# Optimization experiments

Measured on AMD Instinct MI355X. Metric: run time of the kernel, lower is better.

Reference implementation:

```python
import jax, jax.numpy as jnp
import numpy as np

IN_F, OUT_F = 4096, 11008
IN_G, OUT_G = 8, 1
NUM_CB, CB_SIZE = 2, 256


def setup_inputs() -> dict:
    key = jax.random.key(0)
    k1, k2, k3, k4, k5 = jax.random.split(key, 5)
    no, ni = OUT_F // OUT_G, IN_F // IN_G
    x = jax.random.normal(k1, (4, 2048, IN_F), dtype=jnp.float32)
    codes = jax.random.randint(k2, (no, ni, NUM_CB), 0, CB_SIZE, dtype=jnp.int32)
    codebooks = jax.random.normal(k3, (NUM_CB, CB_SIZE, OUT_G, IN_G), dtype=jnp.float32)
    scales = jax.random.uniform(k4, (no, 1, 1, 1), dtype=jnp.float32) + 0.5
    bias = jax.random.normal(k5, (OUT_F,), dtype=jnp.float32)
    return {"x": x, "codes": codes, "codebooks": codebooks, "scales": scales, "bias": bias}


def _dequantize_weight(codes, codebooks, scales):
    # codes: [no, ni, M] ints; codebooks: [M, C, og, ig]; scales: [no, 1, 1, 1]
    M = codebooks.shape[0]
    og, ig = codebooks.shape[2], codebooks.shape[3]
    no, ni = codes.shape[0], codes.shape[1]
    # gather each codebook's entry and sum over codebooks -> [no, ni, og, ig]
    m_idx = jnp.arange(M)[None, None, :]
    gathered = codebooks[m_idx, codes]            # [no, ni, M, og, ig]
    deq = gathered.sum(axis=2) * scales           # [no, ni, og, ig]
    # reorder groups back to dense weight [out_features, in_features]
    return deq.transpose(0, 2, 1, 3).reshape(no * og, ni * ig)


def reference(x, codes, codebooks, scales, bias):
    w = _dequantize_weight(codes, codebooks, scales)  # [OUT_F, IN_F]
    return jnp.einsum("bsi,oi->bso", x, w) + bias
```

## Files before the change

kernel.cpp:

```cpp
#include <hip/hip_runtime.h>
#include <hip/hip_bf16.h>
#include <stdint.h>

#define IN_F   4096
#define OUT_F  11008
#define M_TOK  8192

typedef __attribute__((ext_vector_type(4))) int   int32x4;

__global__ __launch_bounds__(256) void k_prep(
        const float* __restrict__ x,
        const int* __restrict__ codes,
        const float* __restrict__ codebooks,
        const float* __restrict__ scales,
        signed char* __restrict__ Xq, float* __restrict__ sx,
        signed char* __restrict__ Wq, float* __restrict__ sw) {
    __shared__ float cb[4096];
    __shared__ float red[256];
    int t = threadIdx.x;

    if (blockIdx.x < M_TOK) {
        int r = blockIdx.x;
        const float4* xr = (const float4*)(x + (size_t)r * IN_F) + t * 4;
        float4 v0 = xr[0], v1 = xr[1], v2 = xr[2], v3 = xr[3];
        float m = 0.f;
#define MX4(v) m = fmaxf(m, fmaxf(fmaxf(fabsf(v.x), fabsf(v.y)), fmaxf(fabsf(v.z), fabsf(v.w))))
        MX4(v0); MX4(v1); MX4(v2); MX4(v3);
        red[t] = m; __syncthreads();
        for (int s = 128; s > 0; s >>= 1) {
            if (t < s) red[t] = fmaxf(red[t], red[t + s]);
            __syncthreads();
        }
        float rm = fmaxf(red[0], 1e-8f);
        if (t == 0) sx[r] = rm / 127.f;
        float inv = 127.f / rm;
        union { signed char c[16]; uint4 u; } pk;
#define Q4(v, o) pk.c[o] = (signed char)__float2int_rn(v.x * inv);            \
                 pk.c[o+1] = (signed char)__float2int_rn(v.y * inv);          \
                 pk.c[o+2] = (signed char)__float2int_rn(v.z * inv);          \
                 pk.c[o+3] = (signed char)__float2int_rn(v.w * inv)
        Q4(v0, 0); Q4(v1, 4); Q4(v2, 8); Q4(v3, 12);
        *(uint4*)(Xq + (size_t)r * IN_F + t * 16) = pk.u;
    } else {
        int o = blockIdx.x - M_TOK;
        {
            const float4* cbg = (const float4*)codebooks;
            float4* cbl = (float4*)cb;
#pragma unroll
            for (int i = 0; i < 4; ++i) cbl[t + i * 256] = cbg[t + i * 256];
        }
        __syncthreads();
        const int2* cp = (const int2*)codes + (size_t)o * 512 + t * 2;
        int2 c0 = cp[0], c1 = cp[1];
        float e[16]; float m = 0.f;
#pragma unroll
        for (int j = 0; j < 8; ++j) {
            e[j]     = cb[c0.x * 8 + j] + cb[2048 + c0.y * 8 + j];
            e[8 + j] = cb[c1.x * 8 + j] + cb[2048 + c1.y * 8 + j];
        }
#pragma unroll
        for (int j = 0; j < 16; ++j) m = fmaxf(m, fabsf(e[j]));
        red[t] = m; __syncthreads();
        for (int s = 128; s > 0; s >>= 1) {
            if (t < s) red[t] = fmaxf(red[t], red[t + s]);
            __syncthreads();
        }
        float rm = fmaxf(red[0], 1e-8f);
        if (t == 0) sw[o] = scales[o] * rm / 127.f;
        float inv = 127.f / rm;
        union { signed char c[16]; uint4 u; } pk;
#pragma unroll
        for (int j = 0; j < 16; ++j) pk.c[j] = (signed char)__float2int_rn(e[j] * inv);
        *(uint4*)(Wq + (size_t)o * IN_F + t * 16) = pk.u;
    }
}


#define BARRIER() __builtin_amdgcn_s_barrier()
#define VMW(n)    asm volatile("s_waitcnt vmcnt(" #n ")")

#define GL16(gp, lp) __builtin_amdgcn_global_load_lds(                        \
    (const __attribute__((address_space(1))) void*)(gp),                      \
    (__attribute__((address_space(3))) void*)(lp), 16, 0, 0)

__global__ __launch_bounds__(512, 2) void k_gemm(
        const signed char* __restrict__ A,
        const signed char* __restrict__ B,
        const float* __restrict__ sx,
        const float* __restrict__ sw,
        const float* __restrict__ bias,
        float* __restrict__ out) {
    __shared__ signed char lA0[256 * 128];
    __shared__ signed char lA1[256 * 128];
    __shared__ signed char lB0[256 * 128];
    __shared__ signed char lB1[256 * 128];

    const int tid = threadIdx.x;
    const int l = tid & 63;
    const int w = tid >> 6;
    const int wm = w >> 2, wn = w & 3;

    int lid = blockIdx.x;
    int xcd = lid & 7, j = lid >> 3;
    int bx = j >> 2;
    int by = (xcd << 2) + (j & 3);
    const int rowBase = by * 256;
    const int colBase = bx * 256;

    const int srow = w * 8 + (l >> 3);
    const int scol = ((l & 7) ^ ((l >> 3) & 7)) << 4;
    const signed char* gA = A + (size_t)(rowBase + srow) * IN_F + scol;
    const signed char* gB = B + (size_t)(colBase + srow) * IN_F + scol;
    signed char* lA0w = &lA0[w * 8 * 128];
    signed char* lA1w = &lA1[w * 8 * 128];
    signed char* lB0w = &lB0[w * 8 * 128];
    signed char* lB1w = &lB1[w * 8 * 128];

#define STAGEQ_(P, t, q) do {                                                 \
    const signed char* _g = (((q) < 2) ? gA : gB) + (size_t)(t) * 128;        \
    signed char* _l = (((q) < 2) ? lA##P##w : lB##P##w);                      \
    const int _r = ((q) & 1) * 128;                                           \
    GL16(_g + (size_t)_r * IN_F,        _l + _r * 128);                       \
    GL16(_g + (size_t)(_r + 64) * IN_F, _l + (_r + 64) * 128);                \
} while (0)

    const int frow = l & 15, g = l >> 4;
    const int cho0 = ((g ^ (frow & 7)) << 4);
    const int cho1 = (((4 + g) ^ (frow & 7)) << 4);
    const char* rowA0 = (const char*)&lA0[(wm * 128 + frow) * 128];
    const char* rowA1 = (const char*)&lA1[(wm * 128 + frow) * 128];
    const char* rowB0 = (const char*)&lB0[(wn * 64 + frow) * 128];
    const char* rowB1 = (const char*)&lB1[(wn * 64 + frow) * 128];
#define LDA_(P, m, kk) (*(const int32x4*)(rowA##P + (m) * 2048 + ((kk) ? cho1 : cho0)))
#define LDB_(P, n, kk) (*(const int32x4*)(rowB##P + (n) * 2048 + ((kk) ? cho1 : cho0)))

    int32x4 acc[8][4] = {};
    int32x4 ar[4][2], br[4][2];

#define QUAD(M0, N0) do {                                                     \
    _Pragma("unroll") for (int mm = 0; mm < 4; ++mm)                          \
    _Pragma("unroll") for (int nn = 0; nn < 2; ++nn)                          \
    _Pragma("unroll") for (int kk = 0; kk < 2; ++kk)                          \
        acc[(M0) + mm][(N0) + nn] = __builtin_amdgcn_mfma_i32_16x16x64_i8(    \
            ar[mm][kk], br[(N0) + nn][kk], acc[(M0) + mm][(N0) + nn], 0, 0, 0);\
} while (0)

#define RD_A03_B01(P) do {                                                    \
    _Pragma("unroll") for (int mm = 0; mm < 4; ++mm) {                        \
        ar[mm][0] = LDA_(P, mm, 0); ar[mm][1] = LDA_(P, mm, 1); }             \
    br[0][0] = LDB_(P, 0, 0); br[0][1] = LDB_(P, 0, 1);                       \
    br[1][0] = LDB_(P, 1, 0); br[1][1] = LDB_(P, 1, 1);                       \
} while (0)
#define RD_B23(P) do {                                                        \
    br[2][0] = LDB_(P, 2, 0); br[2][1] = LDB_(P, 2, 1);                       \
    br[3][0] = LDB_(P, 3, 0); br[3][1] = LDB_(P, 3, 1);                       \
} while (0)
#define RD_A47(P) do {                                                        \
    _Pragma("unroll") for (int mm = 0; mm < 4; ++mm) {                        \
        ar[mm][0] = LDA_(P, 4 + mm, 0); ar[mm][1] = LDA_(P, 4 + mm, 1); }     \
} while (0)

    STAGEQ_(0, 0, 0); STAGEQ_(0, 0, 1); STAGEQ_(0, 0, 2); STAGEQ_(0, 0, 3);
    STAGEQ_(1, 1, 2); STAGEQ_(1, 1, 3); STAGEQ_(1, 1, 0); STAGEQ_(1, 1, 1);
    VMW(8); BARRIER();

    for (int i = 0; i < 15; ++i) {
        int t = 2 * i;
        RD_A03_B01(0);
        QUAD(0, 0); BARRIER();
        RD_B23(0);
        QUAD(0, 2); BARRIER();
        RD_A47(0); STAGEQ_(0, t + 2, 2); STAGEQ_(0, t + 2, 3);
        QUAD(4, 2); BARRIER();
        STAGEQ_(0, t + 2, 0); STAGEQ_(0, t + 2, 1); VMW(8);
        QUAD(4, 0); BARRIER();
        RD_A03_B01(1);
        QUAD(0, 0); BARRIER();
        RD_B23(1);
        QUAD(0, 2); BARRIER();
        RD_A47(1); STAGEQ_(1, t + 3, 2); STAGEQ_(1, t + 3, 3);
        QUAD(4, 2); BARRIER();
        STAGEQ_(1, t + 3, 0); STAGEQ_(1, t + 3, 1); VMW(8);
        QUAD(4, 0); BARRIER();
    }

    RD_A03_B01(0);
    QUAD(0, 0); BARRIER();
    RD_B23(0);
    QUAD(0, 2); BARRIER();
    RD_A47(0);
    QUAD(4, 2); BARRIER();
    VMW(0);
    QUAD(4, 0); BARRIER();
    RD_A03_B01(1);
    QUAD(0, 0); BARRIER();
    RD_B23(1);
    QUAD(0, 2); BARRIER();
    RD_A47(1);
    QUAD(4, 2); BARRIER();
    QUAD(4, 0);

#pragma unroll
    for (int n = 0; n < 4; ++n) {
        int gcol = colBase + wn * 64 + n * 16 + frow;
        float swv = sw[gcol];
        float bv = bias[gcol];
#pragma unroll
        for (int m = 0; m < 8; ++m) {
            int grow0 = rowBase + wm * 128 + m * 16 + g * 4;
            float4 sx4 = *(const float4*)&sx[grow0];
            out[(size_t)(grow0 + 0) * OUT_F + gcol] = (float)acc[m][n][0] * sx4.x * swv + bv;
            out[(size_t)(grow0 + 1) * OUT_F + gcol] = (float)acc[m][n][1] * sx4.y * swv + bv;
            out[(size_t)(grow0 + 2) * OUT_F + gcol] = (float)acc[m][n][2] * sx4.z * swv + bv;
            out[(size_t)(grow0 + 3) * OUT_F + gcol] = (float)acc[m][n][3] * sx4.w * swv + bv;
        }
    }
}

extern "C" void kernel_launch(void* const* d_in, const int* in_sizes, int n_in,
                              void* d_out, int out_size, void* d_ws, size_t ws_size,
                              hipStream_t stream) {
    const float* x         = (const float*)d_in[0];
    const int*   codes     = (const int*)d_in[1];
    const float* codebooks = (const float*)d_in[2];
    const float* scales    = (const float*)d_in[3];
    const float* bias      = (const float*)d_in[4];
    float* out = (float*)d_out;

    signed char* Wq = (signed char*)d_ws;
    signed char* Xq = Wq + (size_t)OUT_F * IN_F;
    float* sx = (float*)(Xq + (size_t)M_TOK * IN_F);
    float* sw = sx + M_TOK;

    k_prep<<<M_TOK + OUT_F, 256, 0, stream>>>(x, codes, codebooks, scales,
                                              Xq, sx, Wq, sw);
    k_gemm<<<1376, 512, 0, stream>>>(Xq, Wq, sx, sw, bias, out);
}
```

Baseline: 458.1 us.

## Switch int8 GEMM to 32x32x32 MFMA with half-tile staging schedule

Replaces the 16x16x64 int8 MFMA tiling with 32x32x32 MFMA instructions, so each wave holds a 4x2 grid of 32x32 accumulators. This cuts the LDS fragment reads per unit of math. The global-to-LDS staging is restructured into half-tile (A or B) chunks that are interleaved with compute, using fewer barriers per k-step. The epilogue is remapped to the 32x32 output register layout. The risks are register pressure from int32x16 accumulators and the more complex ordering of the double-buffer hazards.

```diff
diff --git a/kernel.cpp b/kernel.cpp
--- a/kernel.cpp
+++ b/kernel.cpp
@@ -6,7 +6,8 @@
 #define OUT_F  11008
 #define M_TOK  8192
 
-typedef __attribute__((ext_vector_type(4))) int   int32x4;
+typedef __attribute__((ext_vector_type(4)))  int int32x4;
+typedef __attribute__((ext_vector_type(16))) int int32x16;
 
 __global__ __launch_bounds__(256) void k_prep(
         const float* __restrict__ x,
@@ -116,103 +117,106 @@
     signed char* lB0w = &lB0[w * 8 * 128];
     signed char* lB1w = &lB1[w * 8 * 128];
 
-#define STAGEQ_(P, t, q) do {                                                 \
-    const signed char* _g = (((q) < 2) ? gA : gB) + (size_t)(t) * 128;        \
-    signed char* _l = (((q) < 2) ? lA##P##w : lB##P##w);                      \
-    const int _r = ((q) & 1) * 128;                                           \
-    GL16(_g + (size_t)_r * IN_F,        _l + _r * 128);                       \
-    GL16(_g + (size_t)(_r + 64) * IN_F, _l + (_r + 64) * 128);                \
-} while (0)
-
-    const int frow = l & 15, g = l >> 4;
-    const int cho0 = ((g ^ (frow & 7)) << 4);
-    const int cho1 = (((4 + g) ^ (frow & 7)) << 4);
-    const char* rowA0 = (const char*)&lA0[(wm * 128 + frow) * 128];
-    const char* rowA1 = (const char*)&lA1[(wm * 128 + frow) * 128];
-    const char* rowB0 = (const char*)&lB0[(wn * 64 + frow) * 128];
-    const char* rowB1 = (const char*)&lB1[(wn * 64 + frow) * 128];
-#define LDA_(P, m, kk) (*(const int32x4*)(rowA##P + (m) * 2048 + ((kk) ? cho1 : cho0)))
-#define LDB_(P, n, kk) (*(const int32x4*)(rowB##P + (n) * 2048 + ((kk) ? cho1 : cho0)))
-
-    int32x4 acc[8][4] = {};
-    int32x4 ar[4][2], br[4][2];
-
-#define QUAD(M0, N0) do {                                                     \
-    _Pragma("unroll") for (int mm = 0; mm < 4; ++mm)                          \
+#define STAGEH_(P, t, H) do {                                                 \
+    const signed char* _g = ((H) ? gB : gA) + (size_t)(t) * 128;              \
+    signed char* _l = ((H) ? lB##P##w : lA##P##w);                            \
+    GL16(_g,                       _l);                                       \
+    GL16(_g +  64 * IN_F,          _l +  64 * 128);                           \
+    GL16(_g + 128 * IN_F,          _l + 128 * 128);                           \
+    GL16(_g + 192 * IN_F,          _l + 192 * 128);                           \
+} while (0)
+
+    const int fr32 = l & 31, hi = l >> 5;
+    const int cho0 = (((0 * 2 + hi) ^ (l & 7)) << 4);
+    const int cho1 = (((1 * 2 + hi) ^ (l & 7)) << 4);
+    const int cho2 = (((2 * 2 + hi) ^ (l & 7)) << 4);
+    const int cho3 = (((3 * 2 + hi) ^ (l & 7)) << 4);
+#define CHO(kk) ((kk) == 0 ? cho0 : (kk) == 1 ? cho1 : (kk) == 2 ? cho2 : cho3)
+    const char* rowA0 = (const char*)&lA0[(wm * 128 + fr32) * 128];
+    const char* rowA1 = (const char*)&lA1[(wm * 128 + fr32) * 128];
+    const char* rowB0 = (const char*)&lB0[(wn * 64 + fr32) * 128];
+    const char* rowB1 = (const char*)&lB1[(wn * 64 + fr32) * 128];
+#define LDA_(P, m, kk) (*(const int32x4*)(rowA##P + (m) * 4096 + CHO(kk)))
+#define LDB_(P, n, kk) (*(const int32x4*)(rowB##P + (n) * 4096 + CHO(kk)))
+
+    int32x16 acc[4][2] = {};
+    int32x4 ar[2][4];
+    int32x4 br[2][4];
+
+#define QUAD32(M0) do {                                                       \
+    _Pragma("unroll") for (int mm = 0; mm < 2; ++mm)                          \
     _Pragma("unroll") for (int nn = 0; nn < 2; ++nn)                          \
-    _Pragma("unroll") for (int kk = 0; kk < 2; ++kk)                          \
-        acc[(M0) + mm][(N0) + nn] = __builtin_amdgcn_mfma_i32_16x16x64_i8(    \
-            ar[mm][kk], br[(N0) + nn][kk], acc[(M0) + mm][(N0) + nn], 0, 0, 0);\
-} while (0)
-
-#define RD_A03_B01(P) do {                                                    \
-    _Pragma("unroll") for (int mm = 0; mm < 4; ++mm) {                        \
-        ar[mm][0] = LDA_(P, mm, 0); ar[mm][1] = LDA_(P, mm, 1); }             \
-    br[0][0] = LDB_(P, 0, 0); br[0][1] = LDB_(P, 0, 1);                       \
-    br[1][0] = LDB_(P, 1, 0); br[1][1] = LDB_(P, 1, 1);                       \
-} while (0)
-#define RD_B23(P) do {                                                        \
-    br[2][0] = LDB_(P, 2, 0); br[2][1] = LDB_(P, 2, 1);                       \
-    br[3][0] = LDB_(P, 3, 0); br[3][1] = LDB_(P, 3, 1);                       \
-} while (0)
-#define RD_A47(P) do {                                                        \
-    _Pragma("unroll") for (int mm = 0; mm < 4; ++mm) {                        \
-        ar[mm][0] = LDA_(P, 4 + mm, 0); ar[mm][1] = LDA_(P, 4 + mm, 1); }     \
-} while (0)
-
-    STAGEQ_(0, 0, 0); STAGEQ_(0, 0, 1); STAGEQ_(0, 0, 2); STAGEQ_(0, 0, 3);
-    STAGEQ_(1, 1, 2); STAGEQ_(1, 1, 3); STAGEQ_(1, 1, 0); STAGEQ_(1, 1, 1);
-    VMW(8); BARRIER();
+    _Pragma("unroll") for (int kk = 0; kk < 4; ++kk)                          \
+        acc[(M0) + mm][nn] = __builtin_amdgcn_mfma_i32_32x32x32_i8(           \
+            ar[mm][kk], br[nn][kk], acc[(M0) + mm][nn], 0, 0, 0);             \
+} while (0)
+
+#define RD_AR01(P) do {                                                       \
+    _Pragma("unroll") for (int mm = 0; mm < 2; ++mm)                          \
+    _Pragma("unroll") for (int kk = 0; kk < 4; ++kk)                          \
+        ar[mm][kk] = LDA_(P, mm, kk);                                         \
+} while (0)
+#define RD_AR23(P) do {                                                       \
+    _Pragma("unroll") for (int mm = 0; mm < 2; ++mm)                          \
+    _Pragma("unroll") for (int kk = 0; kk < 4; ++kk)                          \
+        ar[mm][kk] = LDA_(P, 2 + mm, kk);                                     \
+} while (0)
+#define RD_BR(P) do {                                                         \
+    _Pragma("unroll") for (int nn = 0; nn < 2; ++nn)                          \
+    _Pragma("unroll") for (int kk = 0; kk < 4; ++kk)                          \
+        br[nn][kk] = LDB_(P, nn, kk);                                         \
+} while (0)
+
+    STAGEH_(0, 0, 0); STAGEH_(0, 0, 1);
+    STAGEH_(1, 1, 1);
+    VMW(4); BARRIER();
 
     for (int i = 0; i < 15; ++i) {
-        int t = 2 * i;
-        RD_A03_B01(0);
-        QUAD(0, 0); BARRIER();
-        RD_B23(0);
-        QUAD(0, 2); BARRIER();
-        RD_A47(0); STAGEQ_(0, t + 2, 2); STAGEQ_(0, t + 2, 3);
-        QUAD(4, 2); BARRIER();
-        STAGEQ_(0, t + 2, 0); STAGEQ_(0, t + 2, 1); VMW(8);
-        QUAD(4, 0); BARRIER();
-        RD_A03_B01(1);
-        QUAD(0, 0); BARRIER();
-        RD_B23(1);
-        QUAD(0, 2); BARRIER();
-        RD_A47(1); STAGEQ_(1, t + 3, 2); STAGEQ_(1, t + 3, 3);
-        QUAD(4, 2); BARRIER();
-        STAGEQ_(1, t + 3, 0); STAGEQ_(1, t + 3, 1); VMW(8);
-        QUAD(4, 0); BARRIER();
+        int e = 2 * i, o = 2 * i + 1;
+        RD_AR01(0); RD_BR(0);
+        STAGEH_(1, o, 0);
+        QUAD32(0); BARRIER();
+        RD_AR23(0);
+        STAGEH_(0, e + 2, 1);
+        QUAD32(2);
+        VMW(4); BARRIER();
+        RD_AR01(1); RD_BR(1);
+        STAGEH_(0, e + 2, 0);
+        QUAD32(0); BARRIER();
+        RD_AR23(1);
+        STAGEH_(1, o + 2, 1);
+        QUAD32(2);
+        VMW(4); BARRIER();
     }
 
-    RD_A03_B01(0);
-    QUAD(0, 0); BARRIER();
-    RD_B23(0);
-    QUAD(0, 2); BARRIER();
-    RD_A47(0);
-    QUAD(4, 2); BARRIER();
-    VMW(0);
-    QUAD(4, 0); BARRIER();
-    RD_A03_B01(1);
-    QUAD(0, 0); BARRIER();
-    RD_B23(1);
-    QUAD(0, 2); BARRIER();
-    RD_A47(1);
-    QUAD(4, 2); BARRIER();
-    QUAD(4, 0);
-
-#pragma unroll
-    for (int n = 0; n < 4; ++n) {
-        int gcol = colBase + wn * 64 + n * 16 + frow;
+    RD_AR01(0); RD_BR(0);
+    STAGEH_(1, 31, 0);
+    QUAD32(0); BARRIER();
+    RD_AR23(0);
+    QUAD32(2);
+    VMW(0); BARRIER();
+    RD_AR01(1); RD_BR(1);
+    QUAD32(0); BARRIER();
+    RD_AR23(1);
+    QUAD32(2);
+
+#pragma unroll
+    for (int n = 0; n < 2; ++n) {
+        int gcol = colBase + wn * 64 + n * 32 + fr32;
         float swv = sw[gcol];
         float bv = bias[gcol];
 #pragma unroll
-        for (int m = 0; m < 8; ++m) {
-            int grow0 = rowBase + wm * 128 + m * 16 + g * 4;
-            float4 sx4 = *(const float4*)&sx[grow0];
-            out[(size_t)(grow0 + 0) * OUT_F + gcol] = (float)acc[m][n][0] * sx4.x * swv + bv;
-            out[(size_t)(grow0 + 1) * OUT_F + gcol] = (float)acc[m][n][1] * sx4.y * swv + bv;
-            out[(size_t)(grow0 + 2) * OUT_F + gcol] = (float)acc[m][n][2] * sx4.z * swv + bv;
-            out[(size_t)(grow0 + 3) * OUT_F + gcol] = (float)acc[m][n][3] * sx4.w * swv + bv;
+        for (int m = 0; m < 4; ++m) {
+            int rbase = rowBase + wm * 128 + m * 32 + 4 * hi;
+#pragma unroll
+            for (int r1 = 0; r1 < 4; ++r1) {
+                int grow0 = rbase + 8 * r1;
+                float4 sx4 = *(const float4*)&sx[grow0];
+                out[(size_t)(grow0 + 0) * OUT_F + gcol] = (float)acc[m][n][r1 * 4 + 0] * sx4.x * swv + bv;
+                out[(size_t)(grow0 + 1) * OUT_F + gcol] = (float)acc[m][n][r1 * 4 + 1] * sx4.y * swv + bv;
+                out[(size_t)(grow0 + 2) * OUT_F + gcol] = (float)acc[m][n][r1 * 4 + 2] * sx4.z * swv + bv;
+                out[(size_t)(grow0 + 3) * OUT_F + gcol] = (float)acc[m][n][r1 * 4 + 3] * sx4.w * swv + bv;
+            }
         }
     }
 }
```

After: 517.3 us. 12.9% more time.
